# Performance work log

Measured on AMD Instinct MI355X. Metric: run time of the kernel, lower is better.

Reference implementation:

```python
import jax, jax.numpy as jnp
import numpy as np

# ---- constants derived exactly as in CQCCExtractor.__init__ ----
SR = 16000
FMIN = 32.7
N_BINS = 96
BINS_OCT = 24
N_CQCC = 20
HOP = 128
Q = 1.0 / (2.0 ** (1.0 / BINS_OCT) - 1.0)
MIN_WIN = max(16, int(Q * SR / FMIN))          # 16699
N_FFT = 1
while N_FFT < MIN_WIN * 2:
    N_FFT <<= 1                                # 65536
NUM_FREQ = N_FFT // 2 + 1                      # 32769


def _dct_mat():
    k = np.arange(N_CQCC)[:, None]
    n = np.arange(N_BINS)[None, :]
    return jnp.asarray(np.cos(np.pi * k * (2 * n + 1) / (2 * N_BINS)), dtype=jnp.float32)


def _delta(feat, N=2):
    # vectorized version of the per-frame python loop: d[t] = sum_n n*(f[min(t+n,T-1)] - f[max(t-n,0)]) / denom
    denom = 2 * sum(i * i for i in range(1, N + 1))
    T = feat.shape[0]
    p = jnp.concatenate([jnp.repeat(feat[:1], N, axis=0), feat, jnp.repeat(feat[-1:], N, axis=0)], axis=0)
    num = sum(n * (p[N + n:N + n + T] - p[N - n:N - n + T]) for n in range(1, N + 1))
    return num / denom


def setup_inputs() -> dict:
    key = jax.random.key(0)
    wav = jax.random.normal(key, (262144,), dtype=jnp.float32)
    return {"wav": wav}


def reference(wav) -> jnp.ndarray:
    # periodic hann window of length MIN_WIN, zero-padded (centered) to N_FFT like torch.stft
    w = 0.5 - 0.5 * jnp.cos(2.0 * jnp.pi * jnp.arange(MIN_WIN, dtype=jnp.float32) / MIN_WIN)
    left = (N_FFT - MIN_WIN) // 2
    win = jnp.zeros((N_FFT,), dtype=jnp.float32).at[left:left + MIN_WIN].set(w)

    # torch.stft(center=True, pad_mode='reflect')
    pad = N_FFT // 2
    x = jnp.pad(wav, pad, mode='reflect')
    n_frames = 1 + wav.shape[0] // HOP
    starts = jnp.arange(n_frames) * HOP
    frames = x[starts[:, None] + jnp.arange(N_FFT)[None, :]] * win      # [T, n_fft]
    spec = jnp.fft.rfft(frames, axis=-1)                                 # [T, F] complex64
    power = jnp.abs(spec) ** 2                                           # [T, F]

    # linear interpolation of STFT power at geometrically spaced CQT freqs
    cqt_freqs = FMIN * 2.0 ** (jnp.arange(N_BINS, dtype=jnp.float32) / BINS_OCT)
    idx_float = cqt_freqs / (SR / 2) * (NUM_FREQ - 1)
    idx_lo = jnp.clip(idx_float.astype(jnp.int32), 0, NUM_FREQ - 2)
    idx_hi = idx_lo + 1
    alpha = (idx_float - idx_lo.astype(jnp.float32))                     # [n_bins]
    cqt_power = (1.0 - alpha) * power[:, idx_lo] + alpha * power[:, idx_hi]  # [T, n_bins]

    log_cqt = jnp.log(jnp.maximum(cqt_power, 1e-8))
    cqcc = log_cqt @ _dct_mat().T                                        # [T, n_cqcc]
    # normalize over time (torch.std default is unbiased, ddof=1)
    cqcc = (cqcc - cqcc.mean(axis=0)) / (jnp.std(cqcc, axis=0, ddof=1) + 1e-8)

    d1 = _delta(cqcc)
    d2 = _delta(d1)
    return jnp.concatenate([cqcc, d1, d2], axis=-1)                      # [T, 3*n_cqcc]
```

## Files before the change

kernel.cpp:

```cpp
#include <hip/hip_runtime.h>
#include <math.h>

#define WAV_N     262144
#define HOP       128
#define MIN_WIN   16699
#define LEFT      24418
#define T_FRAMES  2049
#define N_BINS    96
#define N_CQCC    20
#define F_COMP    192
#define NF        576
#define NBLK      2179
#define NBP       2240
#define PARTLEN   59
#define FULLBLK   130
#define XS_VALID  278843
#define TWOPI     6.283185307179586f

#define BT   32
#define FTW  32
#define AST  36

#define WS_QFP  0
#define WS_V    20643840
#define WS_CQ   30117888
#define WS_SUMS 30281808
#define VTP     2056

__device__ __forceinline__ void f_to_fi_sigma(int f, int& fi, int& sigma) {
    int plane = f / 192;
    int c = f - plane * 192;
    int bin = c >> 1, hi = c & 1;
    float e    = (float)bin / 24.0f;
    float fb   = 32.7f * exp2f(e);
    float idxf = fb / 8000.0f * 32768.0f;
    fi = (int)idxf + hi;
    sigma = (plane == 0) ? 0 : (plane == 1 ? 1 : -1);
}

__global__ __launch_bounds__(256) void k_chunk(const float* __restrict__ wav,
                                               float4* __restrict__ QFP) {
    __shared__ __align__(16) float A_lds[128 * AST];
    int tid = threadIdx.x;
    int b0 = blockIdx.x * BT;
    int f0 = blockIdx.y * FTW;

    {
        int sbase = 128 * b0;
        #pragma unroll
        for (int k = 0; k < 16; ++k) {
            int m = k * 256 + tid;
            int j = m & 127, bl = m >> 7;
            int s = sbase + m;
            float v = 0.0f;
            if (s < XS_VALID) {
                int w = s - 8350;
                if (w < 0) w = -w;
                if (w >= WAV_N) w = 2 * WAV_N - 2 - w;
                v = wav[w];
            }
            A_lds[j * AST + bl] = v;
        }
    }

    int f  = f0 + (tid & 31);
    int bg = tid >> 5;
    int bl0 = bg * 4;
    int bb = b0 + bl0;

    int fi, sg;
    f_to_fi_sigma(f, fi, sg);

    float Dr, Di;
    {
        float fr = (float)fi * (1.0f / 65536.0f) - (float)sg * (1.0f / (float)MIN_WIN);
        fr -= rintf(fr);
        float sn, cs; __sincosf(TWOPI * fr, &sn, &cs);
        Dr = cs; Di = -sn;
    }
    float Wr = 1.0f, Wi = 0.0f;

    float xr[4] = {0, 0, 0, 0}, xi[4] = {0, 0, 0, 0};
    float pr[4], pi[4];

    __syncthreads();

    #pragma unroll 4
    for (int j = 0; j < PARTLEN; ++j) {
        float4 a = *(const float4*)&A_lds[j * AST + bl0];
        const float aa[4] = {a.x, a.y, a.z, a.w};
        #pragma unroll
        for (int i = 0; i < 4; ++i) {
            xr[i] = fmaf(aa[i], Wr, xr[i]);
            xi[i] = fmaf(aa[i], Wi, xi[i]);
        }
        float wr = Wr;
        Wr = wr * Dr - Wi * Di;
        Wi = wr * Di + Wi * Dr;
    }
    #pragma unroll
    for (int i = 0; i < 4; ++i) { pr[i] = xr[i]; pi[i] = xi[i]; }
    #pragma unroll 4
    for (int j = PARTLEN; j < 128; ++j) {
        float4 a = *(const float4*)&A_lds[j * AST + bl0];
        const float aa[4] = {a.x, a.y, a.z, a.w};
        #pragma unroll
        for (int i = 0; i < 4; ++i) {
            xr[i] = fmaf(aa[i], Wr, xr[i]);
            xi[i] = fmaf(aa[i], Wi, xi[i]);
        }
        float wr = Wr;
        Wr = wr * Dr - Wi * Di;
        Wi = wr * Di + Wi * Dr;
    }

    float4* dst = QFP + (size_t)f * NBP + bb;
    #pragma unroll
    for (int i = 0; i < 4; ++i) {
        int b = bb + i;
        unsigned ph = ((unsigned)fi * (unsigned)(LEFT + 128 * b)) & 65535u;
        float frf = (float)ph * (1.0f / 65536.0f)
                  - (float)sg * (float)((128 * b) % MIN_WIN) * (1.0f / (float)MIN_WIN);
        frf -= rintf(frf);
        float sn, cs; __sincosf(TWOPI * frf, &sn, &cs);
        dst[i] = make_float4(xr[i] * cs + xi[i] * sn,
                             xi[i] * cs - xr[i] * sn,
                             pr[i] * cs + pi[i] * sn,
                             pi[i] * cs - pr[i] * sn);
    }
}

#define SEG 5
__global__ __launch_bounds__(512) void k_scan(const float4* __restrict__ QFP,
                                              float2* __restrict__ V,
                                              double* __restrict__ sums) {
    __shared__ float4 col[NBLK];
    __shared__ double2 wsum[8];
    int tid = threadIdx.x;
    int f = blockIdx.x;
    if (f == 0 && tid < 40) sums[tid] = 0.0;

    const float4* g = QFP + (size_t)f * NBP;
    #pragma unroll
    for (int k = 0; k < SEG; ++k) {
        int idx = k * 512 + tid;
        if (idx < NBLK) col[idx] = g[idx];
    }
    __syncthreads();

    int s0 = tid * SEG, s1 = min(s0 + SEG, NBLK);
    double sr = 0.0, si = 0.0;
    for (int i = s0; i < s1; ++i) { sr += col[i].x; si += col[i].y; }
    double r = sr, im = si;
    #pragma unroll
    for (int off = 1; off < 64; off <<= 1) {
        double prx = __shfl_up(r, off);
        double piy = __shfl_up(im, off);
        if ((tid & 63) >= off) { r += prx; im += piy; }
    }
    if ((tid & 63) == 63) wsum[tid >> 6] = make_double2(r, im);
    __syncthreads();
    double basr = 0.0, basi = 0.0;
    int w = tid >> 6;
    for (int ww = 0; ww < w; ++ww) { basr += wsum[ww].x; basi += wsum[ww].y; }
    double gr = basr + r - sr, gi = basi + im - si;
    for (int i = s0; i < s1; ++i) {
        float qx = col[i].x, qy = col[i].y;
        col[i].x = (float)gr; col[i].y = (float)gi;
        gr += qx; gi += qy;
    }
    __syncthreads();

    int fi_, sg_; f_to_fi_sigma(f, fi_, sg_);
    float2* vrow = V + (size_t)f * VTP;
    #pragma unroll
    for (int k = 0; k < SEG; ++k) {
        int t = k * 512 + tid;
        if (t < T_FRAMES) {
            float4 ca = col[t];
            float4 cb = col[t + FULLBLK];
            float ur = cb.x - ca.x + cb.z;
            float ui = cb.y - ca.y + cb.w;
            unsigned ph = ((unsigned)fi_ * 128u * (unsigned)t) & 65535u;
            float frf = (float)ph * (1.0f / 65536.0f)
                      - (float)sg_ * (float)((128 * t) % MIN_WIN) * (1.0f / (float)MIN_WIN);
            frf -= rintf(frf);
            float sn, cs;
            __sincosf(TWOPI * frf, &sn, &cs);
            vrow[t] = make_float2(ur * cs - ui * sn, ur * sn + ui * cs);
        }
    }
}

#define TF 8
__global__ __launch_bounds__(256) void k_cqt(const float2* __restrict__ V,
                                             float* __restrict__ cq,
                                             double* __restrict__ sums) {
    __shared__ float dctm[N_CQCC * N_BINS];
    __shared__ float2 sc[F_COMP * TF];
    __shared__ float lg[N_BINS * TF];
    __shared__ float cqv[N_CQCC * TF];
    int tid = threadIdx.x;
    int tb = blockIdx.x * TF;
    for (int idx = tid; idx < N_CQCC * N_BINS; idx += 256) {
        int k = idx / N_BINS, b = idx - k * N_BINS;
        dctm[idx] = cosf((float)M_PI * (float)(k * (2 * b + 1)) / 192.0f);
    }
    for (int idx = tid; idx < F_COMP * TF; idx += 256) {
        int c = idx / TF, tl = idx % TF;
        int t = tb + tl;
        float2 v = make_float2(0.f, 0.f);
        if (t < T_FRAMES) {
            float2 v0 = V[(size_t)c * VTP + t];
            float2 v1 = V[(size_t)(192 + c) * VTP + t];
            float2 v2 = V[(size_t)(384 + c) * VTP + t];
            v = make_float2(0.5f * v0.x - 0.25f * (v1.x + v2.x),
                            0.5f * v0.y - 0.25f * (v1.y + v2.y));
        }
        sc[idx] = v;
    }
    __syncthreads();
    for (int idx = tid; idx < N_BINS * TF; idx += 256) {
        int b = idx / TF, tl = idx % TF;
        float2 lo = sc[(2 * b) * TF + tl];
        float2 hi = sc[(2 * b + 1) * TF + tl];
        float pl = lo.x * lo.x + lo.y * lo.y;
        float ph = hi.x * hi.x + hi.y * hi.y;
        float e    = (float)b / 24.0f;
        float fb   = 32.7f * exp2f(e);
        float idxf = fb / 8000.0f * 32768.0f;
        float alpha = idxf - (float)((int)idxf);
        float p = (1.0f - alpha) * pl + alpha * ph;
        lg[idx] = logf(fmaxf(p, 1e-8f));
    }
    __syncthreads();
    for (int idx = tid; idx < N_CQCC * TF; idx += 256) {
        int k = idx / TF, tl = idx % TF;
        int t = tb + tl;
        float s = 0.0f;
        #pragma unroll 4
        for (int b = 0; b < N_BINS; ++b) s += dctm[k * N_BINS + b] * lg[b * TF + tl];
        cqv[idx] = (t < T_FRAMES) ? s : 0.0f;
        if (t < T_FRAMES) cq[t * N_CQCC + k] = s;
    }
    __syncthreads();
    if (tid < N_CQCC) {
        double s1 = 0.0, s2 = 0.0;
        #pragma unroll
        for (int tl = 0; tl < TF; ++tl) {
            if (tb + tl < T_FRAMES) {
                double v = (double)cqv[tid * TF + tl];
                s1 += v; s2 += v * v;
            }
        }
        atomicAdd(&sums[tid], s1);
        atomicAdd(&sums[N_CQCC + tid], s2);
    }
}

__device__ __forceinline__ int clampT(int v) {
    return v < 0 ? 0 : (v > T_FRAMES - 1 ? T_FRAMES - 1 : v);
}

__global__ void k_final(const float* __restrict__ cq, const double* __restrict__ sums,
                        float* __restrict__ out) {
    int gid = blockIdx.x * blockDim.x + threadIdx.x;
    if (gid >= T_FRAMES * N_CQCC) return;
    int t = gid / N_CQCC;
    int k = gid - t * N_CQCC;
    double S1 = sums[k], S2 = sums[N_CQCC + k];
    double md = S1 / (double)T_FRAMES;
    double var = (S2 - S1 * md) / (double)(T_FRAMES - 1);
    double sd = sqrt(var > 0.0 ? var : 0.0);
    float m = (float)md;
    float iv = (float)(1.0 / (sd + 1e-8));
    float cv[9];
    #pragma unroll
    for (int j = 0; j < 9; ++j)
        cv[j] = (cq[clampT(t + j - 4) * N_CQCC + k] - m) * iv;
    float dv[5];
    #pragma unroll
    for (int o = -2; o <= 2; ++o) {
        int p = clampT(t + o);
        int h1 = clampT(p + 1) - t, l1 = clampT(p - 1) - t;
        int h2 = clampT(p + 2) - t, l2 = clampT(p - 2) - t;
        dv[o + 2] = ((cv[h1 + 4] - cv[l1 + 4]) + 2.0f * (cv[h2 + 4] - cv[l2 + 4])) * 0.1f;
    }
    out[t * 60 + k]      = cv[4];
    out[t * 60 + 20 + k] = dv[2];
    out[t * 60 + 40 + k] = (dv[3] - dv[1] + 2.0f * (dv[4] - dv[0])) * 0.1f;
}

extern "C" void kernel_launch(void* const* d_in, const int* in_sizes, int n_in,
                              void* d_out, int out_size, void* d_ws, size_t ws_size,
                              hipStream_t stream) {
    const float* wav = (const float*)d_in[0];
    float* out = (float*)d_out;
    char* ws = (char*)d_ws;
    float4* QFP  = (float4*)(ws + WS_QFP);
    float2* V    = (float2*)(ws + WS_V);
    float*  cq   = (float*)(ws + WS_CQ);
    double* sums = (double*)(ws + WS_SUMS);

    k_chunk<<<dim3(NBP / BT, NF / FTW), 256, 0, stream>>>(wav, QFP);
    k_scan<<<NF, 512, 0, stream>>>(QFP, V, sums);
    k_cqt<<<(T_FRAMES + TF - 1) / TF, 256, 0, stream>>>(V, cq, sums);
    k_final<<<(T_FRAMES * N_CQCC + 255) / 256, 256, 0, stream>>>(cq, sums, out);
}
```

Baseline: 105.0 us.

## Compute two frequency columns per thread in k_chunk to reuse LDS loads

The k_chunk tile changes from 32 blocks by 32 frequencies to 16 blocks by 64 frequencies, with 128 threads per block. Each thread now accumulates two frequencies, at f and f+32, from the same LDS float4 reads, so every loaded sample feeds twice as many FMAs. The aim is to halve LDS traffic per FMA and halve the redundant wav staging per frequency. In exchange each thread holds twice the accumulator registers, and smaller blocks change occupancy.

Result: slower. 108.0 us (+2.9%).

```diff
diff --git a/kernel.cpp b/kernel.cpp
--- a/kernel.cpp
+++ b/kernel.cpp
@@ -17,9 +17,9 @@
 #define XS_VALID  278843
 #define TWOPI     6.283185307179586f
 
-#define BT   32
-#define FTW  32
-#define AST  36
+#define BT   16
+#define FTW  64
+#define AST  20
 
 #define WS_QFP  0
 #define WS_V    20643840
@@ -38,7 +38,14 @@
     sigma = (plane == 0) ? 0 : (plane == 1 ? 1 : -1);
 }
 
-__global__ __launch_bounds__(256) void k_chunk(const float* __restrict__ wav,
+__device__ __forceinline__ void make_rot(int fi, int sg, float& Dr, float& Di) {
+    float fr = (float)fi * (1.0f / 65536.0f) - (float)sg * (1.0f / (float)MIN_WIN);
+    fr -= rintf(fr);
+    float sn, cs; __sincosf(TWOPI * fr, &sn, &cs);
+    Dr = cs; Di = -sn;
+}
+
+__global__ __launch_bounds__(128) void k_chunk(const float* __restrict__ wav,
                                                float4* __restrict__ QFP) {
     __shared__ __align__(16) float A_lds[128 * AST];
     int tid = threadIdx.x;
@@ -49,7 +56,7 @@
         int sbase = 128 * b0;
         #pragma unroll
         for (int k = 0; k < 16; ++k) {
-            int m = k * 256 + tid;
+            int m = k * 128 + tid;
             int j = m & 127, bl = m >> 7;
             int s = sbase + m;
             float v = 0.0f;
@@ -63,25 +70,25 @@
         }
     }
 
-    int f  = f0 + (tid & 31);
+    int fl = tid & 31;
     int bg = tid >> 5;
     int bl0 = bg * 4;
     int bb = b0 + bl0;
 
-    int fi, sg;
-    f_to_fi_sigma(f, fi, sg);
-
-    float Dr, Di;
-    {
-        float fr = (float)fi * (1.0f / 65536.0f) - (float)sg * (1.0f / (float)MIN_WIN);
-        fr -= rintf(fr);
-        float sn, cs; __sincosf(TWOPI * fr, &sn, &cs);
-        Dr = cs; Di = -sn;
-    }
-    float Wr = 1.0f, Wi = 0.0f;
-
-    float xr[4] = {0, 0, 0, 0}, xi[4] = {0, 0, 0, 0};
-    float pr[4], pi[4];
+    int fA = f0 + fl;
+    int fB = fA + 32;
+
+    int fiA, sgA, fiB, sgB;
+    f_to_fi_sigma(fA, fiA, sgA);
+    f_to_fi_sigma(fB, fiB, sgB);
+
+    float DrA, DiA, DrB, DiB;
+    make_rot(fiA, sgA, DrA, DiA);
+    make_rot(fiB, sgB, DrB, DiB);
+    float WrA = 1.0f, WiA = 0.0f, WrB = 1.0f, WiB = 0.0f;
+
+    float xr[2][4] = {{0,0,0,0},{0,0,0,0}}, xi[2][4] = {{0,0,0,0},{0,0,0,0}};
+    float pr[2][4], pi[2][4];
 
     __syncthreads();
 
@@ -91,42 +98,60 @@
         const float aa[4] = {a.x, a.y, a.z, a.w};
         #pragma unroll
         for (int i = 0; i < 4; ++i) {
-            xr[i] = fmaf(aa[i], Wr, xr[i]);
-            xi[i] = fmaf(aa[i], Wi, xi[i]);
-        }
-        float wr = Wr;
-        Wr = wr * Dr - Wi * Di;
-        Wi = wr * Di + Wi * Dr;
-    }
-    #pragma unroll
-    for (int i = 0; i < 4; ++i) { pr[i] = xr[i]; pi[i] = xi[i]; }
+            xr[0][i] = fmaf(aa[i], WrA, xr[0][i]);
+            xi[0][i] = fmaf(aa[i], WiA, xi[0][i]);
+            xr[1][i] = fmaf(aa[i], WrB, xr[1][i]);
+            xi[1][i] = fmaf(aa[i], WiB, xi[1][i]);
+        }
+        float wrA = WrA;
+        WrA = wrA * DrA - WiA * DiA;
+        WiA = wrA * DiA + WiA * DrA;
+        float wrB = WrB;
+        WrB = wrB * DrB - WiB * DiB;
+        WiB = wrB * DiB + WiB * DrB;
+    }
+    #pragma unroll
+    for (int q = 0; q < 2; ++q)
+        #pragma unroll
+        for (int i = 0; i < 4; ++i) { pr[q][i] = xr[q][i]; pi[q][i] = xi[q][i]; }
     #pragma unroll 4
     for (int j = PARTLEN; j < 128; ++j) {
         float4 a = *(const float4*)&A_lds[j * AST + bl0];
         const float aa[4] = {a.x, a.y, a.z, a.w};
         #pragma unroll
         for (int i = 0; i < 4; ++i) {
-            xr[i] = fmaf(aa[i], Wr, xr[i]);
-            xi[i] = fmaf(aa[i], Wi, xi[i]);
-        }
-        float wr = Wr;
-        Wr = wr * Dr - Wi * Di;
-        Wi = wr * Di + Wi * Dr;
-    }
-
-    float4* dst = QFP + (size_t)f * NBP + bb;
-    #pragma unroll
-    for (int i = 0; i < 4; ++i) {
-        int b = bb + i;
-        unsigned ph = ((unsigned)fi * (unsigned)(LEFT + 128 * b)) & 65535u;
-        float frf = (float)ph * (1.0f / 65536.0f)
-                  - (float)sg * (float)((128 * b) % MIN_WIN) * (1.0f / (float)MIN_WIN);
-        frf -= rintf(frf);
-        float sn, cs; __sincosf(TWOPI * frf, &sn, &cs);
-        dst[i] = make_float4(xr[i] * cs + xi[i] * sn,
-                             xi[i] * cs - xr[i] * sn,
-                             pr[i] * cs + pi[i] * sn,
-                             pi[i] * cs - pr[i] * sn);
+            xr[0][i] = fmaf(aa[i], WrA, xr[0][i]);
+            xi[0][i] = fmaf(aa[i], WiA, xi[0][i]);
+            xr[1][i] = fmaf(aa[i], WrB, xr[1][i]);
+            xi[1][i] = fmaf(aa[i], WiB, xi[1][i]);
+        }
+        float wrA = WrA;
+        WrA = wrA * DrA - WiA * DiA;
+        WiA = wrA * DiA + WiA * DrA;
+        float wrB = WrB;
+        WrB = wrB * DrB - WiB * DiB;
+        WiB = wrB * DiB + WiB * DrB;
+    }
+
+    #pragma unroll
+    for (int q = 0; q < 2; ++q) {
+        int f  = q ? fB : fA;
+        int fi = q ? fiB : fiA;
+        int sg = q ? sgB : sgA;
+        float4* dst = QFP + (size_t)f * NBP + bb;
+        #pragma unroll
+        for (int i = 0; i < 4; ++i) {
+            int b = bb + i;
+            unsigned ph = ((unsigned)fi * (unsigned)(LEFT + 128 * b)) & 65535u;
+            float frf = (float)ph * (1.0f / 65536.0f)
+                      - (float)sg * (float)((128 * b) % MIN_WIN) * (1.0f / (float)MIN_WIN);
+            frf -= rintf(frf);
+            float sn, cs; __sincosf(TWOPI * frf, &sn, &cs);
+            dst[i] = make_float4(xr[q][i] * cs + xi[q][i] * sn,
+                                 xi[q][i] * cs - xr[q][i] * sn,
+                                 pr[q][i] * cs + pi[q][i] * sn,
+                                 pi[q][i] * cs - pr[q][i] * sn);
+        }
     }
 }
 
@@ -302,7 +327,7 @@
     float*  cq   = (float*)(ws + WS_CQ);
     double* sums = (double*)(ws + WS_SUMS);
 
-    k_chunk<<<dim3(NBP / BT, NF / FTW), 256, 0, stream>>>(wav, QFP);
+    k_chunk<<<dim3(NBP / BT, NF / FTW), 128, 0, stream>>>(wav, QFP);
     k_scan<<<NF, 512, 0, stream>>>(QFP, V, sums);
     k_cqt<<<(T_FRAMES + TF - 1) / TF, 256, 0, stream>>>(V, cq, sums);
     k_final<<<(T_FRAMES * N_CQCC + 255) / 256, 256, 0, stream>>>(cq, sums, out);
```

## Drop LDS staging in k_chunk; read wav directly with wave-uniform addresses

Applied to the files above, without the earlier changes.

Removes the shared-memory staging of the reflected waveform chunk and the block barrier. Each wave now handles 64 frequencies for one group of 4 blocks, so the sample reads are wave-uniform (readfirstlane) and can be scalar or broadcast loads. Interior blocks skip the reflect/valid checks through a fast path. The tile shape changes from 32x32 to 16x64, which alters grid size and per-block work, and relies on scalar/L1 caching for the repeated sample reads.

Measured after the change: 118.3 us. 1.13x slower.

```diff
diff --git a/kernel.cpp b/kernel.cpp
--- a/kernel.cpp
+++ b/kernel.cpp
@@ -17,9 +17,8 @@
 #define XS_VALID  278843
 #define TWOPI     6.283185307179586f
 
-#define BT   32
-#define FTW  32
-#define AST  36
+#define BT   16
+#define FTW  64
 
 #define WS_QFP  0
 #define WS_V    20643840
@@ -38,80 +37,71 @@
     sigma = (plane == 0) ? 0 : (plane == 1 ? 1 : -1);
 }
 
+__device__ __forceinline__ void make_rot(int fi, int sg, float& Dr, float& Di) {
+    float fr = (float)fi * (1.0f / 65536.0f) - (float)sg * (1.0f / (float)MIN_WIN);
+    fr -= rintf(fr);
+    float sn, cs; __sincosf(TWOPI * fr, &sn, &cs);
+    Dr = cs; Di = -sn;
+}
+
+__device__ __forceinline__ float xs_at(const float* __restrict__ wav, int s) {
+    int w = s - 8350;
+    if (w < 0) w = -w;
+    if (w >= WAV_N) w = 2 * WAV_N - 2 - w;
+    float v = wav[w];
+    return (s < XS_VALID) ? v : 0.0f;
+}
+
+#define STEP(a0_, a1_, a2_, a3_) do {                                   \
+    xr[0] = fmaf((a0_), Wr, xr[0]); xi[0] = fmaf((a0_), Wi, xi[0]);     \
+    xr[1] = fmaf((a1_), Wr, xr[1]); xi[1] = fmaf((a1_), Wi, xi[1]);     \
+    xr[2] = fmaf((a2_), Wr, xr[2]); xi[2] = fmaf((a2_), Wi, xi[2]);     \
+    xr[3] = fmaf((a3_), Wr, xr[3]); xi[3] = fmaf((a3_), Wi, xi[3]);     \
+    float wr_ = Wr;                                                     \
+    Wr = wr_ * Dr - Wi * Di;                                            \
+    Wi = wr_ * Di + Wi * Dr; } while (0)
+
 __global__ __launch_bounds__(256) void k_chunk(const float* __restrict__ wav,
                                                float4* __restrict__ QFP) {
-    __shared__ __align__(16) float A_lds[128 * AST];
     int tid = threadIdx.x;
-    int b0 = blockIdx.x * BT;
+    int bx = blockIdx.x;
+    int b0 = bx * BT;
     int f0 = blockIdx.y * FTW;
 
-    {
-        int sbase = 128 * b0;
-        #pragma unroll
-        for (int k = 0; k < 16; ++k) {
-            int m = k * 256 + tid;
-            int j = m & 127, bl = m >> 7;
-            int s = sbase + m;
-            float v = 0.0f;
-            if (s < XS_VALID) {
-                int w = s - 8350;
-                if (w < 0) w = -w;
-                if (w >= WAV_N) w = 2 * WAV_N - 2 - w;
-                v = wav[w];
-            }
-            A_lds[j * AST + bl] = v;
-        }
-    }
-
-    int f  = f0 + (tid & 31);
-    int bg = tid >> 5;
-    int bl0 = bg * 4;
-    int bb = b0 + bl0;
-
-    int fi, sg;
-    f_to_fi_sigma(f, fi, sg);
-
-    float Dr, Di;
-    {
-        float fr = (float)fi * (1.0f / 65536.0f) - (float)sg * (1.0f / (float)MIN_WIN);
-        fr -= rintf(fr);
-        float sn, cs; __sincosf(TWOPI * fr, &sn, &cs);
-        Dr = cs; Di = -sn;
-    }
+    int fl = tid & 63;
+    int bg = __builtin_amdgcn_readfirstlane(tid >> 6);
+    int bb = b0 + bg * 4;
+
+    int f = f0 + fl;
+    int fi, sg; f_to_fi_sigma(f, fi, sg);
+    float Dr, Di; make_rot(fi, sg, Dr, Di);
     float Wr = 1.0f, Wi = 0.0f;
 
     float xr[4] = {0, 0, 0, 0}, xi[4] = {0, 0, 0, 0};
     float pr[4], pi[4];
 
-    __syncthreads();
-
-    #pragma unroll 4
-    for (int j = 0; j < PARTLEN; ++j) {
-        float4 a = *(const float4*)&A_lds[j * AST + bl0];
-        const float aa[4] = {a.x, a.y, a.z, a.w};
+    if (bx >= 5 && bx <= 131) {
+        const float* xc = wav + (128 * bb - 8350);
+        #pragma unroll 4
+        for (int j = 0; j < PARTLEN; ++j)
+            STEP(xc[j], xc[128 + j], xc[256 + j], xc[384 + j]);
         #pragma unroll
-        for (int i = 0; i < 4; ++i) {
-            xr[i] = fmaf(aa[i], Wr, xr[i]);
-            xi[i] = fmaf(aa[i], Wi, xi[i]);
-        }
-        float wr = Wr;
-        Wr = wr * Dr - Wi * Di;
-        Wi = wr * Di + Wi * Dr;
-    }
-    #pragma unroll
-    for (int i = 0; i < 4; ++i) { pr[i] = xr[i]; pi[i] = xi[i]; }
-    #pragma unroll 4
-    for (int j = PARTLEN; j < 128; ++j) {
-        float4 a = *(const float4*)&A_lds[j * AST + bl0];
-        const float aa[4] = {a.x, a.y, a.z, a.w};
+        for (int i = 0; i < 4; ++i) { pr[i] = xr[i]; pi[i] = xi[i]; }
+        #pragma unroll 4
+        for (int j = PARTLEN; j < 128; ++j)
+            STEP(xc[j], xc[128 + j], xc[256 + j], xc[384 + j]);
+    } else {
+        int sb = 128 * bb;
+        #pragma unroll 4
+        for (int j = 0; j < PARTLEN; ++j)
+            STEP(xs_at(wav, sb + j),       xs_at(wav, sb + 128 + j),
+                 xs_at(wav, sb + 256 + j), xs_at(wav, sb + 384 + j));
         #pragma unroll
-        for (int i = 0; i < 4; ++i) {
-            xr[i] = fmaf(aa[i], Wr, xr[i]);
-            xi[i] = fmaf(aa[i], Wi, xi[i]);
-        }
-        float wr = Wr;
-        Wr = wr * Dr - Wi * Di;
-        Wi = wr * Di + Wi * Dr;
+        for (int i = 0; i < 4; ++i) { pr[i] = xr[i]; pi[i] = xi[i]; }
+        #pragma unroll 4
+        for (int j = PARTLEN; j < 128; ++j)
+            STEP(xs_at(wav, sb + j),       xs_at(wav, sb + 128 + j),
+                 xs_at(wav, sb + 256 + j), xs_at(wav, sb + 384 + j));
     }
 
     float4* dst = QFP + (size_t)f * NBP + bb;
```
